# Kernel optimization log

Measured on AMD Instinct MI355X. Metric: run time of the kernel, lower is better.

The kernel has to match this reference:

```python
import jax, jax.numpy as jnp
import numpy as np

B, S, HID, DEP, DS, NTYPES = 8, 128, 768, 64, 768, 45
NEG = -1000000000.0


def setup_inputs() -> dict:
    key = jax.random.key(0)
    ks = jax.random.split(key, 10)
    sc = lambda fan_in: 1.0 / np.sqrt(fan_in)
    return {
        "h": jax.random.normal(ks[0], (B, S, HID), dtype=jnp.float32),
        "dep_type_matrix": jax.random.randint(ks[1], (B, S, S), 0, NTYPES),
        "dep_emb_table": jax.random.normal(ks[2], (NTYPES, DEP), dtype=jnp.float32),
        # Linear weights stored as [in, out] so y = x @ W + b
        "W1_w": jax.random.normal(ks[3], (HID + DEP, DS), dtype=jnp.float32) * sc(HID + DEP),
        "W1_b": jnp.zeros((DS,), dtype=jnp.float32),
        "W2_w": jax.random.normal(ks[4], (HID + DEP, DS), dtype=jnp.float32) * sc(HID + DEP),
        "W2_b": jnp.zeros((DS,), dtype=jnp.float32),
        "gcn_w": jax.random.normal(ks[5], (HID, HID), dtype=jnp.float32) * sc(HID),
        "gcn_b": jnp.zeros((HID,), dtype=jnp.float32),
        "Wo_w": jax.random.normal(ks[6], (DS, HID), dtype=jnp.float32) * sc(DS),
        "Wo_b": jnp.zeros((HID,), dtype=jnp.float32),
    }


def reference(h, dep_type_matrix, dep_emb_table, W1_w, W1_b, W2_w, W2_b,
              gcn_w, gcn_b, Wo_w, Wo_b):
    adj = dep_type_matrix != 0                       # [B,S,S] bool
    dep_emb = dep_emb_table[dep_type_matrix]          # [B,S,S,DEP]

    # concat([h_i, dep_emb]) @ W1  ==  h_i @ W1[:HID] + dep_emb @ W1[HID:]
    hi_t = jnp.einsum('bid,de->bie', h, W1_w[:HID])[:, :, None, :] \
         + jnp.einsum('bijd,de->bije', dep_emb, W1_w[HID:]) + W1_b   # [B,S,S,DS]
    hj_t = jnp.einsum('bjd,de->bje', h, W2_w[:HID])[:, None, :, :] \
         + jnp.einsum('bijd,de->bije', dep_emb, W2_w[HID:]) + W2_b   # [B,S,S,DS]

    relevance = jnp.sum(hi_t * hj_t, axis=-1)         # [B,S,S]
    masked = jnp.where(adj, relevance, NEG)
    A = jax.nn.softmax(masked, axis=2)                # softmax over j

    h_syn = h
    for _ in range(1):  # num_layers = 1
        aggregated = jnp.einsum('bij,bjd->bid', A, h_syn)
        h_syn = jax.nn.relu(aggregated @ gcn_w + gcn_b)
    return h_syn @ Wo_w + Wo_b
```

## Files before the change

kernel.cpp:

```cpp
#include <hip/hip_runtime.h>
#include <hip/hip_bf16.h>

#define BB 8
#define SS 128
#define HID 768
#define DEP 64
#define DSZ 768
#define NT 45
#define NTP 48
#define NEG -1000000000.0f

typedef short bfv8 __attribute__((ext_vector_type(8)));
typedef float f32x4 __attribute__((ext_vector_type(4)));

__device__ __forceinline__ unsigned short f2bf(float x) {
    unsigned int u; __builtin_memcpy(&u, &x, 4);
    u += 0x7fffu + ((u >> 16) & 1u);
    return (unsigned short)(u >> 16);
}
__device__ __forceinline__ float bf2f(unsigned short h) {
    unsigned int u = ((unsigned int)h) << 16;
    float f; __builtin_memcpy(&f, &u, 4);
    return f;
}

__device__ __forceinline__ void gld16(const unsigned short* gp, unsigned short* lp) {
    typedef __attribute__((address_space(1))) const unsigned int GU;
    typedef __attribute__((address_space(3))) unsigned int LU;
    __builtin_amdgcn_global_load_lds((GU*)(uintptr_t)gp,
                                     (LU*)(unsigned int)(uintptr_t)lp, 16, 0, 0);
}

__global__ __launch_bounds__(256) void convec(
    const float* __restrict__ h, const float* __restrict__ table,
    const float* __restrict__ W1, const float* __restrict__ W2,
    const float* __restrict__ gcn, const float* __restrict__ Wo,
    unsigned short* __restrict__ hHi, unsigned short* __restrict__ hLo,
    unsigned short* __restrict__ WtHi, unsigned short* __restrict__ WtLo,
    unsigned short* __restrict__ gTHi, unsigned short* __restrict__ oTHi,
    unsigned short* __restrict__ Ehi, unsigned short* __restrict__ Elo,
    float* __restrict__ cv) {
    const long WN = (long)DSZ * HID;
    int tr = threadIdx.x >> 5, tc = threadIdx.x & 31;
    int z = blockIdx.z;
    if (z < 4) {
        __shared__ float tile[32][33];
        const float* src = z == 0 ? W1 : z == 1 ? W2 : z == 2 ? gcn : Wo;
        unsigned short* dhi = z == 0 ? WtHi : z == 1 ? WtHi + WN
                            : z == 2 ? gTHi : oTHi;
        unsigned short* dlo = z == 0 ? WtLo : z == 1 ? WtLo + WN : nullptr;
        int r0 = blockIdx.y * 32, c0 = blockIdx.x * 32;
#pragma unroll
        for (int k = 0; k < 4; ++k)
            tile[tr + k * 8][tc] = src[(long)(r0 + tr + k * 8) * 768 + c0 + tc];
        __syncthreads();
#pragma unroll
        for (int k = 0; k < 4; ++k) {
            int i = tr + k * 8, j = tc;
            float v = tile[j][i];
            unsigned short hh = f2bf(v);
            long o = (long)(c0 + i) * 768 + r0 + j;
            dhi[o] = hh;
            if (dlo) dlo[o] = f2bf(v - bf2f(hh));
        }
    } else if (z < 12) {
        if (blockIdx.y >= SS / 32) return;
        int b = z - 4;
        int r0 = blockIdx.y * 32, c0 = blockIdx.x * 32;
        const float* Xb = h + (long)b * SS * HID;
#pragma unroll
        for (int k = 0; k < 4; ++k) {
            int rr = r0 + tr + k * 8, cc = c0 + tc;
            float v = Xb[(long)rr * HID + cc];
            unsigned short hh = f2bf(v);
            long o = (long)b * SS * HID + (long)rr * HID + cc;
            hHi[o] = hh;
            hLo[o] = f2bf(v - bf2f(hh));
        }
    } else {
        if (blockIdx.y >= 2) return;
        int t = blockIdx.y * 24 + blockIdx.x;
        if (t >= NT) return;
        const long EN = (long)NTP * DSZ;
        __shared__ float tl[DEP];
        __shared__ float red[256];
        for (int d = threadIdx.x; d < DEP; d += 256) tl[d] = table[t * DEP + d];
        __syncthreads();
        float dotacc = 0.f;
#pragma unroll
        for (int k = 0; k < 3; ++k) {
            int e = threadIdx.x + k * 256;
            float s1 = 0.f, s2 = 0.f;
            for (int d = 0; d < DEP; ++d) {
                float td = tl[d];
                s1 += td * W1[(HID + d) * DSZ + e];
                s2 += td * W2[(HID + d) * DSZ + e];
            }
            long i0 = (long)t * DSZ + e;
            unsigned short h2 = f2bf(s2), h1 = f2bf(s1);
            Ehi[i0] = h2;      Elo[i0] = f2bf(s2 - bf2f(h2));
            Ehi[EN + i0] = h1; Elo[EN + i0] = f2bf(s1 - bf2f(h1));
            dotacc += s1 * s2;
        }
        red[threadIdx.x] = dotacc;
        __syncthreads();
        for (int w = 128; w >= 1; w >>= 1) {
            if (threadIdx.x < w) red[threadIdx.x] += red[threadIdx.x + w];
            __syncthreads();
        }
        if (threadIdx.x == 0) cv[t] = red[0];
    }
}

__global__ __launch_bounds__(256) void pgemm_direct(
    const unsigned short* __restrict__ hHi, const unsigned short* __restrict__ hLo,
    const unsigned short* __restrict__ WtHi, const unsigned short* __restrict__ WtLo,
    const float* __restrict__ b1, const float* __restrict__ b2,
    unsigned short* __restrict__ Phi, unsigned short* __restrict__ Plo) {
    const long MN = (long)BB * SS * DSZ;
    const long WN = (long)DSZ * HID;
    int which = blockIdx.z;
    int m0 = blockIdx.y * 128, n0 = blockIdx.x * 64;
    const unsigned short* bh = WtHi + (long)which * WN;
    const unsigned short* bl = WtLo + (long)which * WN;
    const float* bias = which ? b2 : b1;
    unsigned short* oh = Phi + (long)which * MN;
    unsigned short* ol = Plo + (long)which * MN;

    __shared__ __align__(16) unsigned short sAh[4096], sAl[4096];
    __shared__ __align__(16) unsigned short sBh[2048], sBl[2048];
    int tid = threadIdx.x, lane = tid & 63, wave = tid >> 6;
    int wr = wave >> 1, wc = wave & 1;
    int q = lane >> 4, r = lane & 15;

    f32x4 acc[4][2];
#pragma unroll
    for (int i = 0; i < 4; ++i)
#pragma unroll
        for (int j = 0; j < 2; ++j) acc[i][j] = (f32x4){0.f, 0.f, 0.f, 0.f};

    int arow0 = tid >> 2, ak0 = (tid & 3) << 3;
    int s1 = tid + 256;
    int arow1 = s1 >> 2, ak1 = (s1 & 3) << 3;
    const unsigned short* aP0 = hHi + (long)(m0 + arow0) * HID + ak0;
    const unsigned short* aP1 = hHi + (long)(m0 + arow1) * HID + ak1;
    const unsigned short* alP0 = hLo + (long)(m0 + arow0) * HID + ak0;
    const unsigned short* alP1 = hLo + (long)(m0 + arow1) * HID + ak1;
    const unsigned short* bP  = bh + (long)(n0 + arow0) * DSZ + ak0;
    const unsigned short* blP = bl + (long)(n0 + arow0) * DSZ + ak0;
    unsigned short* lA0  = sAh + (wave << 9);
    unsigned short* lA1  = sAh + 2048 + (wave << 9);
    unsigned short* lAl0 = sAl + (wave << 9);
    unsigned short* lAl1 = sAl + 2048 + (wave << 9);
    unsigned short* lB   = sBh + (wave << 9);
    unsigned short* lBl  = sBl + (wave << 9);

    int aOff[4], bOff[2];
#pragma unroll
    for (int f = 0; f < 4; ++f) aOff[f] = (wr * 64 + f * 16 + r) * 32 + q * 8;
#pragma unroll
    for (int f = 0; f < 2; ++f) bOff[f] = (wc * 32 + f * 16 + r) * 32 + q * 8;

    for (int k0 = 0; k0 < HID; k0 += 32) {
        __syncthreads();
        gld16(aP0 + k0, lA0);
        gld16(aP1 + k0, lA1);
        gld16(alP0 + k0, lAl0);
        gld16(alP1 + k0, lAl1);
        gld16(bP + k0, lB);
        gld16(blP + k0, lBl);
        __syncthreads();
        bfv8 b0h = *(const bfv8*)(sBh + bOff[0]);
        bfv8 b1h = *(const bfv8*)(sBh + bOff[1]);
        bfv8 b0l = *(const bfv8*)(sBl + bOff[0]);
        bfv8 b1l = *(const bfv8*)(sBl + bOff[1]);
#pragma unroll
        for (int fr = 0; fr < 4; ++fr) {
            bfv8 a_h = *(const bfv8*)(sAh + aOff[fr]);
            bfv8 a_l = *(const bfv8*)(sAl + aOff[fr]);
            acc[fr][0] = __builtin_amdgcn_mfma_f32_16x16x32_bf16(a_h, b0h, acc[fr][0], 0, 0, 0);
            acc[fr][0] = __builtin_amdgcn_mfma_f32_16x16x32_bf16(a_h, b0l, acc[fr][0], 0, 0, 0);
            acc[fr][0] = __builtin_amdgcn_mfma_f32_16x16x32_bf16(a_l, b0h, acc[fr][0], 0, 0, 0);
            acc[fr][1] = __builtin_amdgcn_mfma_f32_16x16x32_bf16(a_h, b1h, acc[fr][1], 0, 0, 0);
            acc[fr][1] = __builtin_amdgcn_mfma_f32_16x16x32_bf16(a_h, b1l, acc[fr][1], 0, 0, 0);
            acc[fr][1] = __builtin_amdgcn_mfma_f32_16x16x32_bf16(a_l, b1h, acc[fr][1], 0, 0, 0);
        }
    }
#pragma unroll
    for (int fr = 0; fr < 4; ++fr) {
        int rr = m0 + wr * 64 + fr * 16 + q * 4;
#pragma unroll
        for (int fc = 0; fc < 2; ++fc) {
            int cc = n0 + wc * 32 + fc * 16 + r;
            float bv = bias[cc];
#pragma unroll
            for (int i = 0; i < 4; ++i) {
                float v = acc[fr][fc][i] + bv;
                unsigned short hh = f2bf(v);
                long o = (long)(rr + i) * DSZ + cc;
                oh[o] = hh;
                ol[o] = f2bf(v - bf2f(hh));
            }
        }
    }
}

__device__ __forceinline__ void mfma_core(
    const unsigned short* __restrict__ ah, const unsigned short* __restrict__ al,
    const unsigned short* __restrict__ bh, const unsigned short* __restrict__ bl,
    float* __restrict__ Cb, int K, int kb, int kend, int ldc, int Nvalid,
    int m0, int n0,
    unsigned short* sAh, unsigned short* sAl,
    unsigned short* sBh, unsigned short* sBl) {
    int tid = threadIdx.x;
    int lane = tid & 63, wave = tid >> 6;
    int wr = wave >> 1, wc = wave & 1;
    int q = lane >> 4, r = lane & 15;

    f32x4 acc[4][4];
#pragma unroll
    for (int i = 0; i < 4; ++i)
#pragma unroll
        for (int j = 0; j < 4; ++j) acc[i][j] = (f32x4){0.f, 0.f, 0.f, 0.f};

    int s0 = tid, s1 = tid + 256;
    int arow0 = s0 >> 2, ak0 = (s0 & 3) << 3;
    int arow1 = s1 >> 2, ak1 = (s1 & 3) << 3;
    const unsigned short* aP0 = ah + (long)(m0 + arow0) * K + ak0;
    const unsigned short* aP1 = ah + (long)(m0 + arow1) * K + ak1;
    bool bok0 = (n0 + arow0) < Nvalid, bok1 = (n0 + arow1) < Nvalid;
    const unsigned short* bP0 = bh + (long)(n0 + arow0) * K + ak0;
    const unsigned short* bP1 = bh + (long)(n0 + arow1) * K + ak1;
    const unsigned short* alP0 = al + (long)(m0 + arow0) * K + ak0;
    const unsigned short* alP1 = al + (long)(m0 + arow1) * K + ak1;
    const unsigned short* blP0 = bl + (long)(n0 + arow0) * K + ak0;
    const unsigned short* blP1 = bl + (long)(n0 + arow1) * K + ak1;
    unsigned short* lA0 = sAh + (wave << 9);
    unsigned short* lA1 = sAh + 2048 + (wave << 9);
    unsigned short* lB0 = sBh + (wave << 9);
    unsigned short* lB1 = sBh + 2048 + (wave << 9);
    unsigned short* lAl0 = sAl + (wave << 9);
    unsigned short* lAl1 = sAl + 2048 + (wave << 9);
    unsigned short* lBl0 = sBl + (wave << 9);
    unsigned short* lBl1 = sBl + 2048 + (wave << 9);

    int aOff[4], bOff[4];
#pragma unroll
    for (int f = 0; f < 4; ++f) {
        aOff[f] = (wr * 64 + f * 16 + r) * 32 + q * 8;
        bOff[f] = (wc * 64 + f * 16 + r) * 32 + q * 8;
    }

    for (int k0 = kb; k0 < kend; k0 += 32) {
        __syncthreads();
        gld16(aP0 + k0, lA0);
        gld16(aP1 + k0, lA1);
        if (bok0) gld16(bP0 + k0, lB0);
        if (bok1) gld16(bP1 + k0, lB1);
        gld16(alP0 + k0, lAl0);
        gld16(alP1 + k0, lAl1);
        if (bok0) gld16(blP0 + k0, lBl0);
        if (bok1) gld16(blP1 + k0, lBl1);
        __syncthreads();

        bfv8 bh_r[4], bl_r[4];
#pragma unroll
        for (int fc = 0; fc < 4; ++fc) {
            bh_r[fc] = *(const bfv8*)(sBh + bOff[fc]);
            bl_r[fc] = *(const bfv8*)(sBl + bOff[fc]);
        }
#pragma unroll
        for (int fr = 0; fr < 4; ++fr) {
            bfv8 a_h = *(const bfv8*)(sAh + aOff[fr]);
            bfv8 a_l = *(const bfv8*)(sAl + aOff[fr]);
#pragma unroll
            for (int fc = 0; fc < 4; ++fc) {
                acc[fr][fc] = __builtin_amdgcn_mfma_f32_16x16x32_bf16(a_h, bh_r[fc], acc[fr][fc], 0, 0, 0);
                acc[fr][fc] = __builtin_amdgcn_mfma_f32_16x16x32_bf16(a_h, bl_r[fc], acc[fr][fc], 0, 0, 0);
                acc[fr][fc] = __builtin_amdgcn_mfma_f32_16x16x32_bf16(a_l, bh_r[fc], acc[fr][fc], 0, 0, 0);
            }
        }
    }
#pragma unroll
    for (int fr = 0; fr < 4; ++fr) {
        int rr = m0 + wr * 64 + fr * 16 + q * 4;
#pragma unroll
        for (int fc = 0; fc < 4; ++fc) {
            int cc = n0 + wc * 64 + fc * 16 + r;
            if (cc < Nvalid) {
#pragma unroll
                for (int i = 0; i < 4; ++i)
                    Cb[(long)(rr + i) * ldc + cc] = acc[fr][fc][i];
            }
        }
    }
}

__global__ __launch_bounds__(256) void uvgram_hg(
    const unsigned short* __restrict__ Phi, const unsigned short* __restrict__ Plo,
    const unsigned short* __restrict__ EtHi, const unsigned short* __restrict__ EtLo,
    float* __restrict__ UVP, float* __restrict__ GP,
    const unsigned short* __restrict__ hHi, const unsigned short* __restrict__ gTHi,
    unsigned short* __restrict__ HGT) {
    const long MN = (long)BB * SS * DSZ;
    const long EN = (long)NTP * DSZ;
    const long UVN = (long)BB * SS * NTP;
    const long BSD = (long)SS * DSZ;
    __shared__ __align__(16) unsigned short smem[16384];
    int id = blockIdx.x;
    if (id < 64) {
        int y = id >> 3, z = id & 7;
        int which = z >> 2, split = z & 3;
        mfma_core(Phi + (long)which * MN, Plo + (long)which * MN,
                  EtHi + (long)which * EN, EtLo + (long)which * EN,
                  UVP + (long)which * 4 * UVN + (long)split * UVN,
                  DSZ, split * 192, split * 192 + 192, NTP, NTP,
                  y * 128, 0, smem, smem + 8192, smem + 4096, smem + 12288);
    } else if (id < 128) {
        int g = id - 64;
        int b = g >> 3, split = g & 7;
        mfma_core(Phi + (long)b * BSD, Plo + (long)b * BSD,
                  Phi + MN + (long)b * BSD, Plo + MN + (long)b * BSD,
                  GP + (long)b * 8 * (SS * SS) + (long)split * (SS * SS),
                  DSZ, split * 96, split * 96 + 96, SS, SS,
                  0, 0, smem, smem + 8192, smem + 4096, smem + 12288);
    } else {
        int hgid = id - 128;
        int n0 = (hgid % 12) * 64, m0 = (hgid / 12) * 64;
        unsigned short* sA = smem;
        unsigned short* sB = smem + 2048;
        int tid = threadIdx.x, lane = tid & 63, wave = tid >> 6;
        int wr = wave >> 1, wc = wave & 1;
        int q = lane >> 4, r = lane & 15;
        f32x4 acc[2][2];
#pragma unroll
        for (int i = 0; i < 2; ++i)
#pragma unroll
            for (int j = 0; j < 2; ++j) acc[i][j] = (f32x4){0.f, 0.f, 0.f, 0.f};
        int arow = tid >> 2, ak = (tid & 3) << 3;
        const unsigned short* aP = hHi + (long)(m0 + arow) * HID + ak;
        const unsigned short* bP = gTHi + (long)(n0 + arow) * HID + ak;
        unsigned short* lA = sA + (wave << 9);
        unsigned short* lB = sB + (wave << 9);
        int aOff[2], bOff[2];
#pragma unroll
        for (int f = 0; f < 2; ++f) {
            aOff[f] = (wr * 32 + f * 16 + r) * 32 + q * 8;
            bOff[f] = (wc * 32 + f * 16 + r) * 32 + q * 8;
        }
        for (int k0 = 0; k0 < HID; k0 += 32) {
            __syncthreads();
            gld16(aP + k0, lA);
            gld16(bP + k0, lB);
            __syncthreads();
            bfv8 b0 = *(const bfv8*)(sB + bOff[0]);
            bfv8 b1 = *(const bfv8*)(sB + bOff[1]);
#pragma unroll
            for (int fr = 0; fr < 2; ++fr) {
                bfv8 a = *(const bfv8*)(sA + aOff[fr]);
                acc[fr][0] = __builtin_amdgcn_mfma_f32_16x16x32_bf16(a, b0, acc[fr][0], 0, 0, 0);
                acc[fr][1] = __builtin_amdgcn_mfma_f32_16x16x32_bf16(a, b1, acc[fr][1], 0, 0, 0);
            }
        }
#pragma unroll
        for (int fr = 0; fr < 2; ++fr) {
            int rr = m0 + wr * 32 + fr * 16 + q * 4;
#pragma unroll
            for (int fc = 0; fc < 2; ++fc) {
                int cc = n0 + wc * 32 + fc * 16 + r;
#pragma unroll
                for (int i = 0; i < 4; ++i) {
                    int m = rr + i;
                    long o = (long)(m >> 7) * ((long)HID * SS) + (long)cc * SS + (m & 127);
                    HGT[o] = f2bf(acc[fr][fc][i]);
                }
            }
        }
    }
}

template <int OUT>
__global__ __launch_bounds__(256) void gemm64(
    const unsigned short* __restrict__ Ahi, const unsigned short* __restrict__ Bhi,
    const float* __restrict__ bias, unsigned short* __restrict__ Chi,
    float* __restrict__ Cf, int relu, int K, int ldc,
    long sA, long sB, long sC) {
    int batch = blockIdx.z;
    int m0 = blockIdx.y * 64, n0 = blockIdx.x * 64;
    const unsigned short* ah = Ahi + (long)batch * sA;
    const unsigned short* bh = Bhi + (long)batch * sB;

    __shared__ __align__(16) unsigned short sAh[2048], sBh[2048];
    int tid = threadIdx.x;
    int lane = tid & 63, wave = tid >> 6;
    int wr = wave >> 1, wc = wave & 1;
    int q = lane >> 4, r = lane & 15;

    f32x4 acc[2][2];
#pragma unroll
    for (int i = 0; i < 2; ++i)
#pragma unroll
        for (int j = 0; j < 2; ++j) acc[i][j] = (f32x4){0.f, 0.f, 0.f, 0.f};

    int arow = tid >> 2, ak = (tid & 3) << 3;
    const unsigned short* aP = ah + (long)(m0 + arow) * K + ak;
    const unsigned short* bP = bh + (long)(n0 + arow) * K + ak;
    unsigned short* lA = sAh + (wave << 9);
    unsigned short* lB = sBh + (wave << 9);

    int aOff[2], bOff[2];
#pragma unroll
    for (int f = 0; f < 2; ++f) {
        aOff[f] = (wr * 32 + f * 16 + r) * 32 + q * 8;
        bOff[f] = (wc * 32 + f * 16 + r) * 32 + q * 8;
    }

    for (int k0 = 0; k0 < K; k0 += 32) {
        __syncthreads();
        gld16(aP + k0, lA);
        gld16(bP + k0, lB);
        __syncthreads();
        bfv8 b0 = *(const bfv8*)(sBh + bOff[0]);
        bfv8 b1 = *(const bfv8*)(sBh + bOff[1]);
#pragma unroll
        for (int fr = 0; fr < 2; ++fr) {
            bfv8 a = *(const bfv8*)(sAh + aOff[fr]);
            acc[fr][0] = __builtin_amdgcn_mfma_f32_16x16x32_bf16(a, b0, acc[fr][0], 0, 0, 0);
            acc[fr][1] = __builtin_amdgcn_mfma_f32_16x16x32_bf16(a, b1, acc[fr][1], 0, 0, 0);
        }
    }
#pragma unroll
    for (int fr = 0; fr < 2; ++fr) {
        int rr = m0 + wr * 32 + fr * 16 + q * 4;
#pragma unroll
        for (int fc = 0; fc < 2; ++fc) {
            int cc = n0 + wc * 32 + fc * 16 + r;
            float bv = bias ? bias[cc] : 0.f;
#pragma unroll
            for (int i = 0; i < 4; ++i) {
                float v = acc[fr][fc][i] + bv;
                if constexpr (OUT == 1) {
                    if (relu) v = fmaxf(v, 0.f);
                    Chi[(long)batch * sC + (long)(rr + i) * ldc + cc] = f2bf(v);
                } else {
                    Cf[(long)batch * sC + (long)(rr + i) * ldc + cc] = v;
                }
            }
        }
    }
}

__global__ __launch_bounds__(128) void softmax_kernel(
    const int* __restrict__ dep, const float* __restrict__ Gp,
    const float* __restrict__ Up, const float* __restrict__ cv,
    unsigned short* __restrict__ Ahi) {
    const long UVN = (long)BB * SS * NTP;
    int bi = blockIdx.x;
    int b = bi >> 7;
    int j = threadIdx.x;
    int t = dep[(long)bi * SS + j];
    float r;
    if (t != 0) {
        long gbase = (long)bi * SS + j + (long)b * 7L * SS * SS;
        float g = 0.f;
        for (int s = 0; s < 8; ++s) g += Gp[gbase + (long)s * (SS * SS)];
        float su = 0.f, sv = 0.f;
        long ui = (long)bi * NTP + t;
        long vi = ((long)b * SS + j) * NTP + t;
        for (int s = 0; s < 4; ++s) {
            su += Up[(long)s * UVN + ui];
            sv += Up[(long)(4 + s) * UVN + vi];
        }
        r = g + su + sv + cv[t];
    } else {
        r = NEG;
    }
    float m = r;
    for (int off = 1; off < 64; off <<= 1) m = fmaxf(m, __shfl_xor(m, off));
    __shared__ float smax[2], ssum[2];
    if ((threadIdx.x & 63) == 0) smax[threadIdx.x >> 6] = m;
    __syncthreads();
    m = fmaxf(smax[0], smax[1]);
    float p = expf(r - m);
    float s = p;
    for (int off = 1; off < 64; off <<= 1) s += __shfl_xor(s, off);
    if ((threadIdx.x & 63) == 0) ssum[threadIdx.x >> 6] = s;
    __syncthreads();
    s = ssum[0] + ssum[1];
    Ahi[(long)bi * SS + j] = f2bf(p / s);
}

__global__ void e_kernel(const float* __restrict__ table,
                         const float* __restrict__ W1,
                         const float* __restrict__ W2,
                         float* __restrict__ Ef) {
    int idx = blockIdx.x * blockDim.x + threadIdx.x;
    if (idx >= NTP * DSZ) return;
    int t = idx / DSZ, e = idx % DSZ;
    float s1 = 0.f, s2 = 0.f;
    if (t < NT)
        for (int d = 0; d < DEP; ++d) {
            float td = table[t * DEP + d];
            s1 += td * W1[(HID + d) * DSZ + e];
            s2 += td * W2[(HID + d) * DSZ + e];
        }
    const long EN = (long)NTP * DSZ;
    Ef[idx] = s2; Ef[EN + idx] = s1;
}

__global__ void c_kernel(const float* __restrict__ Ef, float* __restrict__ cv) {
    int t = blockIdx.x;
    const long EN = (long)NTP * DSZ;
    float s = 0.f;
    for (int e = threadIdx.x; e < DSZ; e += 256)
        s += Ef[(long)t * DSZ + e] * Ef[EN + (long)t * DSZ + e];
    __shared__ float red[256];
    red[threadIdx.x] = s;
    __syncthreads();
    for (int w = 128; w >= 1; w >>= 1) {
        if (threadIdx.x < w) red[threadIdx.x] += red[threadIdx.x + w];
        __syncthreads();
    }
    if (threadIdx.x == 0) cv[t] = red[0];
}

__device__ __forceinline__ void gemm_body(
    const float* __restrict__ Ab, const float* __restrict__ Bb,
    const float* __restrict__ bias, float* __restrict__ Cb,
    int kbeg, int kend, int lda, int ldb, int ldc,
    int row0, int col0, bool relu) {
    __shared__ float As[16][68];
    __shared__ float Bs[16][68];
    int tx = threadIdx.x & 15, ty = threadIdx.x >> 4;
    float acc[4][4] = {};
    for (int k0 = kbeg; k0 < kend; k0 += 16) {
#pragma unroll
        for (int l = 0; l < 4; ++l) {
            int idx = threadIdx.x + l * 256;
            int r = idx >> 4, kk = idx & 15;
            As[kk][r] = Ab[(long)(row0 + r) * lda + k0 + kk];
            int kk2 = idx >> 6, cc = idx & 63;
            Bs[kk2][cc] = Bb[(long)(k0 + kk2) * ldb + col0 + cc];
        }
        __syncthreads();
#pragma unroll
        for (int kk = 0; kk < 16; ++kk) {
            float4 a4 = *(const float4*)&As[kk][ty * 4];
            float4 b4 = *(const float4*)&Bs[kk][tx * 4];
            float a[4] = {a4.x, a4.y, a4.z, a4.w};
            float b[4] = {b4.x, b4.y, b4.z, b4.w};
#pragma unroll
            for (int i = 0; i < 4; ++i)
#pragma unroll
                for (int j = 0; j < 4; ++j) acc[i][j] += a[i] * b[j];
        }
        __syncthreads();
    }
#pragma unroll
    for (int i = 0; i < 4; ++i) {
        int r = row0 + ty * 4 + i;
#pragma unroll
        for (int j = 0; j < 4; ++j) {
            int c = col0 + tx * 4 + j;
            float v = acc[i][j];
            if (bias) v += bias[c];
            if (relu) v = fmaxf(v, 0.f);
            Cb[(long)r * ldc + c] = v;
        }
    }
}

__global__ __launch_bounds__(256) void gemm_k(
// ... 53 lines not shown
    for (int e = threadIdx.x; e < DSZ; e += 256) {
        p1[e] = P1[(long)bs * DSZ + e];
        p2[e] = P2[(long)bs * DSZ + e];
    }
    __syncthreads();
    int wave = threadIdx.x / 64, lane = threadIdx.x % 64;
    for (int t = wave; t < NT; t += 4) {
        float su = 0.f, sv = 0.f;
        for (int e = lane; e < DSZ; e += 64) {
            su += p1[e] * E2[(long)t * DSZ + e];
            sv += p2[e] * E1[(long)t * DSZ + e];
        }
        for (int off = 32; off >= 1; off >>= 1) {
            su += __shfl_down(su, off);
            sv += __shfl_down(sv, off);
        }
        if (lane == 0) {
            U[(long)bs * NTP + t] = su;
            V[(long)bs * NTP + t] = sv + cv[t];
        }
    }
}

__global__ __launch_bounds__(128) void softmax_fb(
    const int* __restrict__ dep, const float* __restrict__ G,
    const float* __restrict__ U, const float* __restrict__ V,
    float* __restrict__ A) {
    int bi = blockIdx.x;
    int b = bi >> 7;
    int j = threadIdx.x;
    int t = dep[(long)bi * SS + j];
    float r;
    if (t != 0)
        r = G[(long)bi * SS + j] + U[(long)bi * NTP + t] + V[((long)b * SS + j) * NTP + t];
    else
        r = NEG;
    float m = r;
    for (int off = 1; off < 64; off <<= 1) m = fmaxf(m, __shfl_xor(m, off));
    __shared__ float smax[2], ssum[2];
    if ((threadIdx.x & 63) == 0) smax[threadIdx.x >> 6] = m;
    __syncthreads();
    m = fmaxf(smax[0], smax[1]);
    float p = expf(r - m);
    float s = p;
    for (int off = 1; off < 64; off <<= 1) s += __shfl_xor(s, off);
    if ((threadIdx.x & 63) == 0) ssum[threadIdx.x >> 6] = s;
    __syncthreads();
    s = ssum[0] + ssum[1];
    A[(long)bi * SS + j] = p / s;
}

extern "C" void kernel_launch(void* const* d_in, const int* in_sizes, int n_in,
                              void* d_out, int out_size, void* d_ws, size_t ws_size,
                              hipStream_t stream) {
    const float* h      = (const float*)d_in[0];
    const int*   dep    = (const int*)d_in[1];
    const float* table  = (const float*)d_in[2];
    const float* W1_w   = (const float*)d_in[3];
    const float* W1_b   = (const float*)d_in[4];
    const float* W2_w   = (const float*)d_in[5];
    const float* W2_b   = (const float*)d_in[6];
    const float* gcn_w  = (const float*)d_in[7];
    const float* gcn_b  = (const float*)d_in[8];
    const float* Wo_w   = (const float*)d_in[9];
    const float* Wo_b   = (const float*)d_in[10];
    float* out = (float*)d_out;

    const long nBS = (long)BB * SS;
    const long MN  = nBS * DSZ;
    const long BSS = (long)BB * SS * SS;
    const long UVN = nBS * NTP;
    const long EN  = (long)NTP * DSZ;
    const long WN  = (long)DSZ * HID;
    const long BSD = (long)SS * DSZ;

    char* base = (char*)d_ws;
    size_t off = 0;
    auto alloc = [&](size_t bytes) -> void* {
        void* p = base + off;
        off += (bytes + 255) & ~(size_t)255;
        return p;
    };

    float* CV    = (float*)alloc(256);
    float* GP    = (float*)alloc(8 * BSS * 4);
    float* UVP   = (float*)alloc(8 * UVN * 4);
    unsigned short* EtHi = (unsigned short*)alloc(2 * EN * 2);
    unsigned short* EtLo = (unsigned short*)alloc(2 * EN * 2);
    unsigned short* hHi  = (unsigned short*)alloc(MN * 2);
    unsigned short* hLo  = (unsigned short*)alloc(MN * 2);
    unsigned short* WtHi = (unsigned short*)alloc(2 * WN * 2);
    unsigned short* WtLo = (unsigned short*)alloc(2 * WN * 2);
    unsigned short* gTHi = (unsigned short*)alloc(WN * 2);
    unsigned short* oTHi = (unsigned short*)alloc(WN * 2);
    unsigned short* Phi  = (unsigned short*)alloc(2 * MN * 2);
    unsigned short* Plo  = (unsigned short*)alloc(2 * MN * 2);
    unsigned short* AmHi = (unsigned short*)alloc(BSS * 2);
    unsigned short* HGT  = (unsigned short*)alloc(MN * 2);
    unsigned short* HSHi = (unsigned short*)alloc(MN * 2);
    size_t needBig = off;

    if (ws_size >= needBig) {
        convec<<<dim3(24, 24, 13), 256, 0, stream>>>(
            h, table, W1_w, W2_w, gcn_w, Wo_w,
            hHi, hLo, WtHi, WtLo, gTHi, oTHi, EtHi, EtLo, CV);
        pgemm_direct<<<dim3(12, 8, 2), 256, 0, stream>>>(
            hHi, hLo, WtHi, WtLo, W1_b, W2_b, Phi, Plo);
        uvgram_hg<<<320, 256, 0, stream>>>(
            Phi, Plo, EtHi, EtLo, UVP, GP, hHi, gTHi, HGT);
        softmax_kernel<<<nBS, 128, 0, stream>>>(dep, GP, UVP, CV, AmHi);
        gemm64<1><<<dim3(12, 2, 8), 256, 0, stream>>>(
            AmHi, HGT, gcn_b, HSHi, nullptr, 1, SS, HID,
            (long)SS * SS, (long)HID * SS, BSD);
        gemm64<2><<<dim3(12, 16, 1), 256, 0, stream>>>(
            HSHi, oTHi, Wo_b, nullptr, out, 0, DSZ, HID, 0, 0, 0);
    } else {
        float* ws = (float*)d_ws;
        long o2 = 0;
        float* Ef2  = ws + o2; o2 += 2 * EN;
        float* CV2  = ws + o2; o2 += 64;
        float* P1   = ws + o2; o2 += MN;
        float* P2   = ws + o2; o2 += MN;
        float* Uf   = ws + o2; o2 += UVN;
        float* Vf   = ws + o2; o2 += UVN;
        float* G    = ws + o2; o2 += BSS;
        float* Amat = ws + o2; o2 += BSS;
        float* AGG  = ws + o2; o2 += MN;
        float* HSYN = ws + o2; o2 += MN;

        e_kernel<<<(NTP * DSZ + 255) / 256, 256, 0, stream>>>(table, W1_w, W2_w, Ef2);
        c_kernel<<<NT, 256, 0, stream>>>(Ef2, CV2);
        gemm_k<<<dim3(DSZ / 64, nBS / 64, 1), 256, 0, stream>>>(
            h, W1_w, W1_b, P1, HID, 1, HID, DSZ, DSZ, 0, 0, 0, 0, 0);
        gemm_k<<<dim3(DSZ / 64, nBS / 64, 1), 256, 0, stream>>>(
            h, W2_w, W2_b, P2, HID, 1, HID, DSZ, DSZ, 0, 0, 0, 0, 0);
        uv_kernel<<<nBS, 256, 0, stream>>>(P1, P2, Ef2 + EN, Ef2, CV2, Uf, Vf);
        gram32<<<dim3(SS / 32, SS / 32, BB), 256, 0, stream>>>(P1, P2, G);
        softmax_fb<<<nBS, 128, 0, stream>>>(dep, G, Uf, Vf, Amat);
        gemm_k<<<dim3(HID / 64, SS / 64, BB), 256, 0, stream>>>(
            Amat, h, nullptr, AGG, SS, 1, SS, HID, HID,
            (long)SS * SS, BSD, BSD, 0, 0);
        gemm_k<<<dim3(HID / 64, nBS / 64, 1), 256, 0, stream>>>(
            AGG, gcn_w, gcn_b, HSYN, HID, 1, HID, HID, HID, 0, 0, 0, 0, 1);
        gemm_k<<<dim3(HID / 64, nBS / 64, 1), 256, 0, stream>>>(
            HSYN, Wo_w, Wo_b, out, DSZ, 1, DSZ, HID, HID, 0, 0, 0, 0, 0);
    }
}
```

Before: 85.33 us.

## Fuse post-convert stages into a persistent megakernel with grid barriers

Replaces five separate kernel launches (projection GEMM, UV/Gram/HG GEMMs, softmax, GCN GEMM, output GEMM) with one persistent kernel sized to the CU count. It loops over work tiles per stage and separates stages with atomic-counter grid barriers. The goal is to remove launch gaps and tail overhead between small dependent kernels. In exchange it adds barrier spin cost, a memset, host device-property queries on every call, and a deadlock risk if not all blocks are co-resident.

```diff
diff --git a/kernel.cpp b/kernel.cpp
--- a/kernel.cpp
+++ b/kernel.cpp
@@ -29,6 +29,18 @@
     typedef __attribute__((address_space(3))) unsigned int LU;
     __builtin_amdgcn_global_load_lds((GU*)(uintptr_t)gp,
                                      (LU*)(unsigned int)(uintptr_t)lp, 16, 0, 0);
+}
+
+__device__ __forceinline__ void gridbar(int* bar, int idx, int GRID) {
+    __syncthreads();
+    if (threadIdx.x == 0) {
+        __threadfence();
+        __hip_atomic_fetch_add(bar + idx, 1, __ATOMIC_ACQ_REL, __HIP_MEMORY_SCOPE_AGENT);
+        while (__hip_atomic_load(bar + idx, __ATOMIC_ACQUIRE, __HIP_MEMORY_SCOPE_AGENT) < GRID)
+            __builtin_amdgcn_s_sleep(1);
+        __threadfence();
+    }
+    __syncthreads();
 }
 
 __global__ __launch_bounds__(256) void convec(
@@ -112,23 +124,24 @@
     }
 }
 
-__global__ __launch_bounds__(256) void pgemm_direct(
+__device__ __forceinline__ void pgemm_body(
     const unsigned short* __restrict__ hHi, const unsigned short* __restrict__ hLo,
     const unsigned short* __restrict__ WtHi, const unsigned short* __restrict__ WtLo,
     const float* __restrict__ b1, const float* __restrict__ b2,
-    unsigned short* __restrict__ Phi, unsigned short* __restrict__ Plo) {
+    unsigned short* __restrict__ Phi, unsigned short* __restrict__ Plo,
+    int which, int m0, int n0, unsigned short* smem) {
     const long MN = (long)BB * SS * DSZ;
     const long WN = (long)DSZ * HID;
-    int which = blockIdx.z;
-    int m0 = blockIdx.y * 128, n0 = blockIdx.x * 64;
     const unsigned short* bh = WtHi + (long)which * WN;
     const unsigned short* bl = WtLo + (long)which * WN;
     const float* bias = which ? b2 : b1;
     unsigned short* oh = Phi + (long)which * MN;
     unsigned short* ol = Plo + (long)which * MN;
 
-    __shared__ __align__(16) unsigned short sAh[4096], sAl[4096];
-    __shared__ __align__(16) unsigned short sBh[2048], sBl[2048];
+    unsigned short* sAh = smem;
+    unsigned short* sAl = smem + 4096;
+    unsigned short* sBh = smem + 8192;
+    unsigned short* sBl = smem + 10240;
     int tid = threadIdx.x, lane = tid & 63, wave = tid >> 6;
     int wr = wave >> 1, wc = wave & 1;
     int q = lane >> 4, r = lane & 15;
@@ -296,101 +309,17 @@
     }
 }
 
-__global__ __launch_bounds__(256) void uvgram_hg(
-    const unsigned short* __restrict__ Phi, const unsigned short* __restrict__ Plo,
-    const unsigned short* __restrict__ EtHi, const unsigned short* __restrict__ EtLo,
-    float* __restrict__ UVP, float* __restrict__ GP,
-    const unsigned short* __restrict__ hHi, const unsigned short* __restrict__ gTHi,
-    unsigned short* __restrict__ HGT) {
-    const long MN = (long)BB * SS * DSZ;
-    const long EN = (long)NTP * DSZ;
-    const long UVN = (long)BB * SS * NTP;
-    const long BSD = (long)SS * DSZ;
-    __shared__ __align__(16) unsigned short smem[16384];
-    int id = blockIdx.x;
-    if (id < 64) {
-        int y = id >> 3, z = id & 7;
-        int which = z >> 2, split = z & 3;
-        mfma_core(Phi + (long)which * MN, Plo + (long)which * MN,
-                  EtHi + (long)which * EN, EtLo + (long)which * EN,
-                  UVP + (long)which * 4 * UVN + (long)split * UVN,
-                  DSZ, split * 192, split * 192 + 192, NTP, NTP,
-                  y * 128, 0, smem, smem + 8192, smem + 4096, smem + 12288);
-    } else if (id < 128) {
-        int g = id - 64;
-        int b = g >> 3, split = g & 7;
-        mfma_core(Phi + (long)b * BSD, Plo + (long)b * BSD,
-                  Phi + MN + (long)b * BSD, Plo + MN + (long)b * BSD,
-                  GP + (long)b * 8 * (SS * SS) + (long)split * (SS * SS),
-                  DSZ, split * 96, split * 96 + 96, SS, SS,
-                  0, 0, smem, smem + 8192, smem + 4096, smem + 12288);
-    } else {
-        int hgid = id - 128;
-        int n0 = (hgid % 12) * 64, m0 = (hgid / 12) * 64;
-        unsigned short* sA = smem;
-        unsigned short* sB = smem + 2048;
-        int tid = threadIdx.x, lane = tid & 63, wave = tid >> 6;
-        int wr = wave >> 1, wc = wave & 1;
-        int q = lane >> 4, r = lane & 15;
-        f32x4 acc[2][2];
-#pragma unroll
-        for (int i = 0; i < 2; ++i)
-#pragma unroll
-            for (int j = 0; j < 2; ++j) acc[i][j] = (f32x4){0.f, 0.f, 0.f, 0.f};
-        int arow = tid >> 2, ak = (tid & 3) << 3;
-        const unsigned short* aP = hHi + (long)(m0 + arow) * HID + ak;
-        const unsigned short* bP = gTHi + (long)(n0 + arow) * HID + ak;
-        unsigned short* lA = sA + (wave << 9);
-        unsigned short* lB = sB + (wave << 9);
-        int aOff[2], bOff[2];
-#pragma unroll
-        for (int f = 0; f < 2; ++f) {
-            aOff[f] = (wr * 32 + f * 16 + r) * 32 + q * 8;
-            bOff[f] = (wc * 32 + f * 16 + r) * 32 + q * 8;
-        }
-        for (int k0 = 0; k0 < HID; k0 += 32) {
-            __syncthreads();
-            gld16(aP + k0, lA);
-            gld16(bP + k0, lB);
-            __syncthreads();
-            bfv8 b0 = *(const bfv8*)(sB + bOff[0]);
-            bfv8 b1 = *(const bfv8*)(sB + bOff[1]);
-#pragma unroll
-            for (int fr = 0; fr < 2; ++fr) {
-                bfv8 a = *(const bfv8*)(sA + aOff[fr]);
-                acc[fr][0] = __builtin_amdgcn_mfma_f32_16x16x32_bf16(a, b0, acc[fr][0], 0, 0, 0);
-                acc[fr][1] = __builtin_amdgcn_mfma_f32_16x16x32_bf16(a, b1, acc[fr][1], 0, 0, 0);
-            }
-        }
-#pragma unroll
-        for (int fr = 0; fr < 2; ++fr) {
-            int rr = m0 + wr * 32 + fr * 16 + q * 4;
-#pragma unroll
-            for (int fc = 0; fc < 2; ++fc) {
-                int cc = n0 + wc * 32 + fc * 16 + r;
-#pragma unroll
-                for (int i = 0; i < 4; ++i) {
-                    int m = rr + i;
-                    long o = (long)(m >> 7) * ((long)HID * SS) + (long)cc * SS + (m & 127);
-                    HGT[o] = f2bf(acc[fr][fc][i]);
-                }
-            }
-        }
-    }
-}
-
 template <int OUT>
-__global__ __launch_bounds__(256) void gemm64(
+__device__ __forceinline__ void gemm64_body(
     const unsigned short* __restrict__ Ahi, const unsigned short* __restrict__ Bhi,
     const float* __restrict__ bias, unsigned short* __restrict__ Chi,
     float* __restrict__ Cf, int relu, int K, int ldc,
-    long sA, long sB, long sC) {
-    int batch = blockIdx.z;
-    int m0 = blockIdx.y * 64, n0 = blockIdx.x * 64;
+    long sA, long sB, long sC, int batch, int m0, int n0,
+    unsigned short* smem) {
     const unsigned short* ah = Ahi + (long)batch * sA;
     const unsigned short* bh = Bhi + (long)batch * sB;
-
-    __shared__ __align__(16) unsigned short sAh[2048], sBh[2048];
+    unsigned short* sAh = smem;
+    unsigned short* sBh = smem + 2048;
     int tid = threadIdx.x;
     int lane = tid & 63, wave = tid >> 6;
     int wr = wave >> 1, wc = wave & 1;
@@ -442,52 +371,122 @@
                 if constexpr (OUT == 1) {
                     if (relu) v = fmaxf(v, 0.f);
                     Chi[(long)batch * sC + (long)(rr + i) * ldc + cc] = f2bf(v);
+                } else if constexpr (OUT == 2) {
+                    Cf[(long)batch * sC + (long)(rr + i) * ldc + cc] = v;
                 } else {
-                    Cf[(long)batch * sC + (long)(rr + i) * ldc + cc] = v;
+                    int m = rr + i;
+                    long o = (long)(m >> 7) * ((long)HID * SS) + (long)cc * SS + (m & 127);
+                    Chi[o] = f2bf(v);
                 }
             }
         }
     }
 }
 
-__global__ __launch_bounds__(128) void softmax_kernel(
-    const int* __restrict__ dep, const float* __restrict__ Gp,
-    const float* __restrict__ Up, const float* __restrict__ cv,
-    unsigned short* __restrict__ Ahi) {
+__global__ __launch_bounds__(256) void mega(
+    const int* __restrict__ dep,
+    const float* __restrict__ b1, const float* __restrict__ b2,
+    const float* __restrict__ gcnb, const float* __restrict__ Wob,
+    float* __restrict__ out, int* bar,
+    const float* __restrict__ CV, float* __restrict__ GP, float* __restrict__ UVP,
+    const unsigned short* __restrict__ EtHi, const unsigned short* __restrict__ EtLo,
+    const unsigned short* __restrict__ hHi, const unsigned short* __restrict__ hLo,
+    const unsigned short* __restrict__ WtHi, const unsigned short* __restrict__ WtLo,
+    const unsigned short* __restrict__ gTHi, const unsigned short* __restrict__ oTHi,
+    unsigned short* __restrict__ Phi, unsigned short* __restrict__ Plo,
+    unsigned short* __restrict__ AmHi, unsigned short* __restrict__ HGT,
+    unsigned short* __restrict__ HSHi, int GRID) {
+    const long MN  = (long)BB * SS * DSZ;
+    const long EN  = (long)NTP * DSZ;
     const long UVN = (long)BB * SS * NTP;
-    int bi = blockIdx.x;
-    int b = bi >> 7;
-    int j = threadIdx.x;
-    int t = dep[(long)bi * SS + j];
-    float r;
-    if (t != 0) {
-        long gbase = (long)bi * SS + j + (long)b * 7L * SS * SS;
-        float g = 0.f;
-        for (int s = 0; s < 8; ++s) g += Gp[gbase + (long)s * (SS * SS)];
-        float su = 0.f, sv = 0.f;
-        long ui = (long)bi * NTP + t;
-        long vi = ((long)b * SS + j) * NTP + t;
-        for (int s = 0; s < 4; ++s) {
-            su += Up[(long)s * UVN + ui];
-            sv += Up[(long)(4 + s) * UVN + vi];
-        }
-        r = g + su + sv + cv[t];
-    } else {
-        r = NEG;
-    }
-    float m = r;
-    for (int off = 1; off < 64; off <<= 1) m = fmaxf(m, __shfl_xor(m, off));
-    __shared__ float smax[2], ssum[2];
-    if ((threadIdx.x & 63) == 0) smax[threadIdx.x >> 6] = m;
-    __syncthreads();
-    m = fmaxf(smax[0], smax[1]);
-    float p = expf(r - m);
-    float s = p;
-    for (int off = 1; off < 64; off <<= 1) s += __shfl_xor(s, off);
-    if ((threadIdx.x & 63) == 0) ssum[threadIdx.x >> 6] = s;
-    __syncthreads();
-    s = ssum[0] + ssum[1];
-    Ahi[(long)bi * SS + j] = f2bf(p / s);
+    const long BSD = (long)SS * DSZ;
+    __shared__ __align__(16) unsigned short smem[16384];
+    int bid = blockIdx.x;
+    int tid = threadIdx.x;
+
+    for (int u = bid; u < 192; u += GRID) {
+        int which = u / 96, v = u % 96;
+        pgemm_body(hHi, hLo, WtHi, WtLo, b1, b2, Phi, Plo,
+                   which, (v / 12) * 128, (v % 12) * 64, smem);
+    }
+    gridbar(bar, 0, GRID);
+
+    for (int u = bid; u < 320; u += GRID) {
+        if (u < 64) {
+            int y = u >> 3, z = u & 7;
+            int which = z >> 2, split = z & 3;
+            mfma_core(Phi + (long)which * MN, Plo + (long)which * MN,
+                      EtHi + (long)which * EN, EtLo + (long)which * EN,
+                      UVP + (long)which * 4 * UVN + (long)split * UVN,
+                      DSZ, split * 192, split * 192 + 192, NTP, NTP,
+                      y * 128, 0, smem, smem + 8192, smem + 4096, smem + 12288);
+        } else if (u < 128) {
+            int g = u - 64;
+            int b = g >> 3, split = g & 7;
+            mfma_core(Phi + (long)b * BSD, Plo + (long)b * BSD,
+                      Phi + MN + (long)b * BSD, Plo + MN + (long)b * BSD,
+                      GP + (long)b * 8 * (SS * SS) + (long)split * (SS * SS),
+                      DSZ, split * 96, split * 96 + 96, SS, SS,
+                      0, 0, smem, smem + 8192, smem + 4096, smem + 12288);
+        } else {
+            int hgid = u - 128;
+            gemm64_body<4>(hHi, gTHi, nullptr, HGT, nullptr, 0, HID, HID,
+                           0, 0, 0, 0, (hgid / 12) * 64, (hgid % 12) * 64, smem);
+        }
+    }
+    gridbar(bar, 1, GRID);
+
+    for (int u = bid; u < 512; u += GRID) {
+        int bi = (u << 1) + (tid >> 7);
+        int j = tid & 127;
+        int b = bi >> 7;
+        int t = dep[(long)bi * SS + j];
+        float r;
+        if (t != 0) {
+            long gbase = (long)bi * SS + j + (long)b * 7L * SS * SS;
+            float g = 0.f;
+            for (int s2 = 0; s2 < 8; ++s2) g += GP[gbase + (long)s2 * (SS * SS)];
+            float su = 0.f, sv = 0.f;
+            long ui = (long)bi * NTP + t;
+            long vi = ((long)b * SS + j) * NTP + t;
+            for (int s2 = 0; s2 < 4; ++s2) {
+                su += UVP[(long)s2 * UVN + ui];
+                sv += UVP[(long)(4 + s2) * UVN + vi];
+            }
+            r = g + su + sv + CV[t];
+        } else {
+            r = NEG;
+        }
+        float* sh = (float*)smem;
+        int wave = tid >> 6, half = tid >> 7;
+        float m = r;
+        for (int off = 1; off < 64; off <<= 1) m = fmaxf(m, __shfl_xor(m, off));
+        if ((tid & 63) == 0) sh[wave] = m;
+        __syncthreads();
+        m = fmaxf(sh[half * 2], sh[half * 2 + 1]);
+        float p = expf(r - m);
+        float s = p;
+        for (int off = 1; off < 64; off <<= 1) s += __shfl_xor(s, off);
+        if ((tid & 63) == 0) sh[4 + wave] = s;
+        __syncthreads();
+        s = sh[half * 2 + 4] + sh[half * 2 + 5];
+        AmHi[(long)bi * SS + j] = f2bf(p / s);
+        __syncthreads();
+    }
+    gridbar(bar, 2, GRID);
+
+    for (int u = bid; u < 192; u += GRID) {
+        int b = u / 24, v = u % 24;
+        gemm64_body<1>(AmHi, HGT, gcnb, HSHi, nullptr, 1, SS, HID,
+                       (long)SS * SS, (long)HID * SS, BSD,
+                       b, (v / 12) * 64, (v % 12) * 64, smem);
+    }
+    gridbar(bar, 3, GRID);
+
+    for (int u = bid; u < 192; u += GRID) {
+        gemm64_body<2>(HSHi, oTHi, Wob, nullptr, out, 0, DSZ, HID,
+                       0, 0, 0, 0, (u / 12) * 64, (u % 12) * 64, smem);
+    }
 }
 
 __global__ void e_kernel(const float* __restrict__ table,
@@ -707,6 +706,7 @@
         return p;
     };
 
+    int*   BAR   = (int*)alloc(256);
     float* CV    = (float*)alloc(256);
     float* GP    = (float*)alloc(8 * BSS * 4);
     float* UVP   = (float*)alloc(8 * UVN * 4);
@@ -726,19 +726,22 @@
     size_t needBig = off;
 
     if (ws_size >= needBig) {
+        int grid = 256;
+        int dev = 0;
+        if (hipGetDevice(&dev) == hipSuccess) {
+            hipDeviceProp_t prop;
+            if (hipGetDeviceProperties(&prop, dev) == hipSuccess &&
+                prop.multiProcessorCount > 0 && prop.multiProcessorCount < 256)
+                grid = prop.multiProcessorCount;
+        }
+        hipMemsetAsync(BAR, 0, 256, stream);
         convec<<<dim3(24, 24, 13), 256, 0, stream>>>(
             h, table, W1_w, W2_w, gcn_w, Wo_w,
             hHi, hLo, WtHi, WtLo, gTHi, oTHi, EtHi, EtLo, CV);
-        pgemm_direct<<<dim3(12, 8, 2), 256, 0, stream>>>(
-            hHi, hLo, WtHi, WtLo, W1_b, W2_b, Phi, Plo);
-        uvgram_hg<<<320, 256, 0, stream>>>(
-            Phi, Plo, EtHi, EtLo, UVP, GP, hHi, gTHi, HGT);
-        softmax_kernel<<<nBS, 128, 0, stream>>>(dep, GP, UVP, CV, AmHi);
-        gemm64<1><<<dim3(12, 2, 8), 256, 0, stream>>>(
-            AmHi, HGT, gcn_b, HSHi, nullptr, 1, SS, HID,
-            (long)SS * SS, (long)HID * SS, BSD);
-        gemm64<2><<<dim3(12, 16, 1), 256, 0, stream>>>(
-            HSHi, oTHi, Wo_b, nullptr, out, 0, DSZ, HID, 0, 0, 0);
+        mega<<<grid, 256, 0, stream>>>(
+            dep, W1_b, W2_b, gcn_b, Wo_b, out, BAR, CV, GP, UVP,
+            EtHi, EtLo, hHi, hLo, WtHi, WtLo, gTHi, oTHi,
+            Phi, Plo, AmHi, HGT, HSHi, grid);
     } else {
         float* ws = (float*)d_ws;
         long o2 = 0;
```

After: 260.9 us. 206% more time.

## Double-buffer LDS staging in all MFMA GEMM loops to overlap loads

Applied to the files above, without the earlier changes.

Each GEMM main loop now issues the direct-to-LDS global loads for the next K tile into a second shared-memory buffer before computing on the current one. One barrier per iteration replaces the previous two, and the mfma_core helper now takes a single smem base pointer. This aims to hide global-load latency behind the MFMA work. In exchange, shared memory per block doubles, which may reduce occupancy. It also relies on gld16 completion being covered by the single barrier.

```diff
diff --git a/kernel.cpp b/kernel.cpp
--- a/kernel.cpp
+++ b/kernel.cpp
@@ -127,8 +127,8 @@
     unsigned short* oh = Phi + (long)which * MN;
     unsigned short* ol = Plo + (long)which * MN;
 
-    __shared__ __align__(16) unsigned short sAh[4096], sAl[4096];
-    __shared__ __align__(16) unsigned short sBh[2048], sBl[2048];
+    __shared__ __align__(16) unsigned short sAh[8192], sAl[8192];
+    __shared__ __align__(16) unsigned short sBh[4096], sBl[4096];
     int tid = threadIdx.x, lane = tid & 63, wave = tid >> 6;
     int wr = wave >> 1, wc = wave & 1;
     int q = lane >> 4, r = lane & 15;
@@ -148,12 +148,6 @@
     const unsigned short* alP1 = hLo + (long)(m0 + arow1) * HID + ak1;
     const unsigned short* bP  = bh + (long)(n0 + arow0) * DSZ + ak0;
     const unsigned short* blP = bl + (long)(n0 + arow0) * DSZ + ak0;
-    unsigned short* lA0  = sAh + (wave << 9);
-    unsigned short* lA1  = sAh + 2048 + (wave << 9);
-    unsigned short* lAl0 = sAl + (wave << 9);
-    unsigned short* lAl1 = sAl + 2048 + (wave << 9);
-    unsigned short* lB   = sBh + (wave << 9);
-    unsigned short* lBl  = sBl + (wave << 9);
 
     int aOff[4], bOff[2];
 #pragma unroll
@@ -161,23 +155,36 @@
 #pragma unroll
     for (int f = 0; f < 2; ++f) bOff[f] = (wc * 32 + f * 16 + r) * 32 + q * 8;
 
+    auto stage = [&](int k0, int db) {
+        unsigned short* a = sAh + db * 4096;
+        unsigned short* al_ = sAl + db * 4096;
+        unsigned short* b = sBh + db * 2048;
+        unsigned short* bl_ = sBl + db * 2048;
+        gld16(aP0 + k0, a + (wave << 9));
+        gld16(aP1 + k0, a + 2048 + (wave << 9));
+        gld16(alP0 + k0, al_ + (wave << 9));
+        gld16(alP1 + k0, al_ + 2048 + (wave << 9));
+        gld16(bP + k0, b + (wave << 9));
+        gld16(blP + k0, bl_ + (wave << 9));
+    };
+
+    stage(0, 0);
+    __syncthreads();
+    int db = 0;
     for (int k0 = 0; k0 < HID; k0 += 32) {
-        __syncthreads();
-        gld16(aP0 + k0, lA0);
-        gld16(aP1 + k0, lA1);
-        gld16(alP0 + k0, lAl0);
-        gld16(alP1 + k0, lAl1);
-        gld16(bP + k0, lB);
-        gld16(blP + k0, lBl);
-        __syncthreads();
-        bfv8 b0h = *(const bfv8*)(sBh + bOff[0]);
-        bfv8 b1h = *(const bfv8*)(sBh + bOff[1]);
-        bfv8 b0l = *(const bfv8*)(sBl + bOff[0]);
-        bfv8 b1l = *(const bfv8*)(sBl + bOff[1]);
+        if (k0 + 32 < HID) stage(k0 + 32, db ^ 1);
+        const unsigned short* cAh = sAh + db * 4096;
+        const unsigned short* cAl = sAl + db * 4096;
+        const unsigned short* cBh = sBh + db * 2048;
+        const unsigned short* cBl = sBl + db * 2048;
+        bfv8 b0h = *(const bfv8*)(cBh + bOff[0]);
+        bfv8 b1h = *(const bfv8*)(cBh + bOff[1]);
+        bfv8 b0l = *(const bfv8*)(cBl + bOff[0]);
+        bfv8 b1l = *(const bfv8*)(cBl + bOff[1]);
 #pragma unroll
         for (int fr = 0; fr < 4; ++fr) {
-            bfv8 a_h = *(const bfv8*)(sAh + aOff[fr]);
-            bfv8 a_l = *(const bfv8*)(sAl + aOff[fr]);
+            bfv8 a_h = *(const bfv8*)(cAh + aOff[fr]);
+            bfv8 a_l = *(const bfv8*)(cAl + aOff[fr]);
             acc[fr][0] = __builtin_amdgcn_mfma_f32_16x16x32_bf16(a_h, b0h, acc[fr][0], 0, 0, 0);
             acc[fr][0] = __builtin_amdgcn_mfma_f32_16x16x32_bf16(a_h, b0l, acc[fr][0], 0, 0, 0);
             acc[fr][0] = __builtin_amdgcn_mfma_f32_16x16x32_bf16(a_l, b0h, acc[fr][0], 0, 0, 0);
@@ -185,6 +192,8 @@
             acc[fr][1] = __builtin_amdgcn_mfma_f32_16x16x32_bf16(a_h, b1l, acc[fr][1], 0, 0, 0);
             acc[fr][1] = __builtin_amdgcn_mfma_f32_16x16x32_bf16(a_l, b1h, acc[fr][1], 0, 0, 0);
         }
+        __syncthreads();
+        db ^= 1;
     }
 #pragma unroll
     for (int fr = 0; fr < 4; ++fr) {
@@ -209,9 +218,11 @@
     const unsigned short* __restrict__ ah, const unsigned short* __restrict__ al,
     const unsigned short* __restrict__ bh, const unsigned short* __restrict__ bl,
     float* __restrict__ Cb, int K, int kb, int kend, int ldc, int Nvalid,
-    int m0, int n0,
-    unsigned short* sAh, unsigned short* sAl,
-    unsigned short* sBh, unsigned short* sBl) {
+    int m0, int n0, unsigned short* smem) {
+    unsigned short* sAh = smem;
+    unsigned short* sAl = smem + 8192;
+    unsigned short* sBh = smem + 16384;
+    unsigned short* sBl = smem + 24576;
     int tid = threadIdx.x;
     int lane = tid & 63, wave = tid >> 6;
     int wr = wave >> 1, wc = wave & 1;
@@ -235,14 +246,6 @@
     const unsigned short* alP1 = al + (long)(m0 + arow1) * K + ak1;
     const unsigned short* blP0 = bl + (long)(n0 + arow0) * K + ak0;
     const unsigned short* blP1 = bl + (long)(n0 + arow1) * K + ak1;
-    unsigned short* lA0 = sAh + (wave << 9);
-    unsigned short* lA1 = sAh + 2048 + (wave << 9);
-    unsigned short* lB0 = sBh + (wave << 9);
-    unsigned short* lB1 = sBh + 2048 + (wave << 9);
-    unsigned short* lAl0 = sAl + (wave << 9);
-    unsigned short* lAl1 = sAl + 2048 + (wave << 9);
-    unsigned short* lBl0 = sBl + (wave << 9);
-    unsigned short* lBl1 = sBl + 2048 + (wave << 9);
 
     int aOff[4], bOff[4];
 #pragma unroll
@@ -251,28 +254,40 @@
         bOff[f] = (wc * 64 + f * 16 + r) * 32 + q * 8;
     }
 
+    auto stage = [&](int k0, int db) {
+        unsigned short* a = sAh + db * 4096;
+        unsigned short* al_ = sAl + db * 4096;
+        unsigned short* b = sBh + db * 4096;
+        unsigned short* bl_ = sBl + db * 4096;
+        gld16(aP0 + k0, a + (wave << 9));
+        gld16(aP1 + k0, a + 2048 + (wave << 9));
+        gld16(alP0 + k0, al_ + (wave << 9));
+        gld16(alP1 + k0, al_ + 2048 + (wave << 9));
+        if (bok0) gld16(bP0 + k0, b + (wave << 9));
+        if (bok1) gld16(bP1 + k0, b + 2048 + (wave << 9));
+        if (bok0) gld16(blP0 + k0, bl_ + (wave << 9));
+        if (bok1) gld16(blP1 + k0, bl_ + 2048 + (wave << 9));
+    };
+
+    stage(kb, 0);
+    __syncthreads();
+    int db = 0;
     for (int k0 = kb; k0 < kend; k0 += 32) {
-        __syncthreads();
-        gld16(aP0 + k0, lA0);
-        gld16(aP1 + k0, lA1);
-        if (bok0) gld16(bP0 + k0, lB0);
-        if (bok1) gld16(bP1 + k0, lB1);
-        gld16(alP0 + k0, lAl0);
-        gld16(alP1 + k0, lAl1);
-        if (bok0) gld16(blP0 + k0, lBl0);
-        if (bok1) gld16(blP1 + k0, lBl1);
-        __syncthreads();
-
+        if (k0 + 32 < kend) stage(k0 + 32, db ^ 1);
+        const unsigned short* cAh = sAh + db * 4096;
+        const unsigned short* cAl = sAl + db * 4096;
+        const unsigned short* cBh = sBh + db * 4096;
+        const unsigned short* cBl = sBl + db * 4096;
         bfv8 bh_r[4], bl_r[4];
 #pragma unroll
         for (int fc = 0; fc < 4; ++fc) {
-            bh_r[fc] = *(const bfv8*)(sBh + bOff[fc]);
-            bl_r[fc] = *(const bfv8*)(sBl + bOff[fc]);
+            bh_r[fc] = *(const bfv8*)(cBh + bOff[fc]);
+            bl_r[fc] = *(const bfv8*)(cBl + bOff[fc]);
         }
 #pragma unroll
         for (int fr = 0; fr < 4; ++fr) {
-            bfv8 a_h = *(const bfv8*)(sAh + aOff[fr]);
-            bfv8 a_l = *(const bfv8*)(sAl + aOff[fr]);
+            bfv8 a_h = *(const bfv8*)(cAh + aOff[fr]);
+            bfv8 a_l = *(const bfv8*)(cAl + aOff[fr]);
 #pragma unroll
             for (int fc = 0; fc < 4; ++fc) {
                 acc[fr][fc] = __builtin_amdgcn_mfma_f32_16x16x32_bf16(a_h, bh_r[fc], acc[fr][fc], 0, 0, 0);
@@ -280,6 +295,8 @@
                 acc[fr][fc] = __builtin_amdgcn_mfma_f32_16x16x32_bf16(a_l, bh_r[fc], acc[fr][fc], 0, 0, 0);
             }
         }
+        __syncthreads();
+        db ^= 1;
     }
 #pragma unroll
     for (int fr = 0; fr < 4; ++fr) {
@@ -306,7 +323,7 @@
     const long EN = (long)NTP * DSZ;
     const long UVN = (long)BB * SS * NTP;
     const long BSD = (long)SS * DSZ;
-    __shared__ __align__(16) unsigned short smem[16384];
+    __shared__ __align__(16) unsigned short smem[32768];
     int id = blockIdx.x;
     if (id < 64) {
         int y = id >> 3, z = id & 7;
@@ -315,7 +332,7 @@
                   EtHi + (long)which * EN, EtLo + (long)which * EN,
                   UVP + (long)which * 4 * UVN + (long)split * UVN,
                   DSZ, split * 192, split * 192 + 192, NTP, NTP,
-                  y * 128, 0, smem, smem + 8192, smem + 4096, smem + 12288);
+                  y * 128, 0, smem);
     } else if (id < 128) {
         int g = id - 64;
         int b = g >> 3, split = g & 7;
@@ -323,12 +340,12 @@
                   Phi + MN + (long)b * BSD, Plo + MN + (long)b * BSD,
                   GP + (long)b * 8 * (SS * SS) + (long)split * (SS * SS),
                   DSZ, split * 96, split * 96 + 96, SS, SS,
-                  0, 0, smem, smem + 8192, smem + 4096, smem + 12288);
+                  0, 0, smem);
     } else {
         int hgid = id - 128;
         int n0 = (hgid % 12) * 64, m0 = (hgid / 12) * 64;
         unsigned short* sA = smem;
-        unsigned short* sB = smem + 2048;
+        unsigned short* sB = smem + 4096;
         int tid = threadIdx.x, lane = tid & 63, wave = tid >> 6;
         int wr = wave >> 1, wc = wave & 1;
         int q = lane >> 4, r = lane & 15;
@@ -340,27 +357,33 @@
         int arow = tid >> 2, ak = (tid & 3) << 3;
         const unsigned short* aP = hHi + (long)(m0 + arow) * HID + ak;
         const unsigned short* bP = gTHi + (long)(n0 + arow) * HID + ak;
-        unsigned short* lA = sA + (wave << 9);
-        unsigned short* lB = sB + (wave << 9);
         int aOff[2], bOff[2];
 #pragma unroll
         for (int f = 0; f < 2; ++f) {
             aOff[f] = (wr * 32 + f * 16 + r) * 32 + q * 8;
             bOff[f] = (wc * 32 + f * 16 + r) * 32 + q * 8;
         }
+        auto stage = [&](int k0, int db) {
+            gld16(aP + k0, sA + db * 2048 + (wave << 9));
+            gld16(bP + k0, sB + db * 2048 + (wave << 9));
+        };
+        stage(0, 0);
+        __syncthreads();
+        int db = 0;
         for (int k0 = 0; k0 < HID; k0 += 32) {
-            __syncthreads();
-            gld16(aP + k0, lA);
-            gld16(bP + k0, lB);
-            __syncthreads();
-            bfv8 b0 = *(const bfv8*)(sB + bOff[0]);
-            bfv8 b1 = *(const bfv8*)(sB + bOff[1]);
+            if (k0 + 32 < HID) stage(k0 + 32, db ^ 1);
+            const unsigned short* cA = sA + db * 2048;
+            const unsigned short* cB = sB + db * 2048;
+            bfv8 b0 = *(const bfv8*)(cB + bOff[0]);
+            bfv8 b1 = *(const bfv8*)(cB + bOff[1]);
 #pragma unroll
             for (int fr = 0; fr < 2; ++fr) {
-                bfv8 a = *(const bfv8*)(sA + aOff[fr]);
+                bfv8 a = *(const bfv8*)(cA + aOff[fr]);
                 acc[fr][0] = __builtin_amdgcn_mfma_f32_16x16x32_bf16(a, b0, acc[fr][0], 0, 0, 0);
                 acc[fr][1] = __builtin_amdgcn_mfma_f32_16x16x32_bf16(a, b1, acc[fr][1], 0, 0, 0);
             }
+            __syncthreads();
+            db ^= 1;
         }
 #pragma unroll
         for (int fr = 0; fr < 2; ++fr) {
@@ -390,7 +413,7 @@
     const unsigned short* ah = Ahi + (long)batch * sA;
     const unsigned short* bh = Bhi + (long)batch * sB;
 
-    __shared__ __align__(16) unsigned short sAh[2048], sBh[2048];
+    __shared__ __align__(16) unsigned short sAh[4096], sBh[4096];
     int tid = threadIdx.x;
     int lane = tid & 63, wave = tid >> 6;
     int wr = wave >> 1, wc = wave & 1;
@@ -405,8 +428,6 @@
     int arow = tid >> 2, ak = (tid & 3) << 3;
     const unsigned short* aP = ah + (long)(m0 + arow) * K + ak;
     const unsigned short* bP = bh + (long)(n0 + arow) * K + ak;
-    unsigned short* lA = sAh + (wave << 9);
-    unsigned short* lB = sBh + (wave << 9);
 
     int aOff[2], bOff[2];
 #pragma unroll
@@ -415,19 +436,27 @@
         bOff[f] = (wc * 32 + f * 16 + r) * 32 + q * 8;
     }
 
+    auto stage = [&](int k0, int db) {
+        gld16(aP + k0, sAh + db * 2048 + (wave << 9));
+        gld16(bP + k0, sBh + db * 2048 + (wave << 9));
+    };
+    stage(0, 0);
+    __syncthreads();
+    int db = 0;
     for (int k0 = 0; k0 < K; k0 += 32) {
-        __syncthreads();
-        gld16(aP + k0, lA);
-        gld16(bP + k0, lB);
-        __syncthreads();
-        bfv8 b0 = *(const bfv8*)(sBh + bOff[0]);
-        bfv8 b1 = *(const bfv8*)(sBh + bOff[1]);
+        if (k0 + 32 < K) stage(k0 + 32, db ^ 1);
+        const unsigned short* cA = sAh + db * 2048;
+        const unsigned short* cB = sBh + db * 2048;
+        bfv8 b0 = *(const bfv8*)(cB + bOff[0]);
+        bfv8 b1 = *(const bfv8*)(cB + bOff[1]);
 #pragma unroll
         for (int fr = 0; fr < 2; ++fr) {
-            bfv8 a = *(const bfv8*)(sAh + aOff[fr]);
+            bfv8 a = *(const bfv8*)(cA + aOff[fr]);
             acc[fr][0] = __builtin_amdgcn_mfma_f32_16x16x32_bf16(a, b0, acc[fr][0], 0, 0, 0);
             acc[fr][1] = __builtin_amdgcn_mfma_f32_16x16x32_bf16(a, b1, acc[fr][1], 0, 0, 0);
         }
+        __syncthreads();
+        db ^= 1;
     }
 #pragma unroll
     for (int fr = 0; fr < 2; ++fr) {
```

New measurement: 74.80 us. 12.3% less time.
